# Kernel tuning notes

Hardware: AMD Instinct MI355X
Metric: run time of the kernel (lower is better)

## Reference

```python
import jax, jax.numpy as jnp
import numpy as np


def setup_inputs() -> dict:
    key = jax.random.key(0)
    k1, k2 = jax.random.split(key)
    B, L, V, D = 8, 2048, 1024, 1024
    hidden_states = jax.random.normal(k1, (B, L, D), dtype=jnp.float32)
    visual_hidden_state = jax.random.normal(k2, (B, V, D), dtype=jnp.float32)
    return {"hidden_states": hidden_states, "visual_hidden_state": visual_hidden_state}


def reference(hidden_states, visual_hidden_state):
    # fusion_scores = H @ V^T  (no scaling, no masking)
    scores = jnp.einsum("bld,bvd->blv", hidden_states, visual_hidden_state)
    probs = jax.nn.softmax(scores, axis=-1)
    # fusion_output = probs @ V
    return jnp.einsum("blv,bvd->bld", probs, visual_hidden_state)
```

## Files before the change

kernel.cpp:

```cpp
#include <hip/hip_runtime.h>


typedef _Float16 half8_t __attribute__((ext_vector_type(8)));
typedef _Float16 half4_t __attribute__((ext_vector_type(4)));
typedef __fp16   fp16x2  __attribute__((ext_vector_type(2)));
typedef float    f32x4   __attribute__((ext_vector_type(4)));

#define B_ 8
#define L_ 2048
#define V_ 1024
#define D_ 1024

__device__ __forceinline__ half8_t cvt8(f32x4 a, f32x4 b) {
  union { half8_t h; fp16x2 p[4]; } u;
  u.p[0] = __builtin_amdgcn_cvt_pkrtz(a[0], a[1]);
  u.p[1] = __builtin_amdgcn_cvt_pkrtz(a[2], a[3]);
  u.p[2] = __builtin_amdgcn_cvt_pkrtz(b[0], b[1]);
  u.p[3] = __builtin_amdgcn_cvt_pkrtz(b[2], b[3]);
  return u.h;
}
__device__ __forceinline__ half4_t cvt4(f32x4 a) {
  union { half4_t h; fp16x2 p[2]; } u;
  u.p[0] = __builtin_amdgcn_cvt_pkrtz(a[0], a[1]);
  u.p[1] = __builtin_amdgcn_cvt_pkrtz(a[2], a[3]);
  return u.h;
}

__device__ __forceinline__ void gload_lds16(const _Float16* g, _Float16* l) {
  __builtin_amdgcn_global_load_lds(
      (const __attribute__((address_space(1))) unsigned int*)(g),
      (__attribute__((address_space(3))) unsigned int*)(l), 16, 0, 0);
}

__global__ __launch_bounds__(256) void p0_hconv(const float* __restrict__ H,
                                                _Float16* __restrict__ Hh) {
  const size_t i = ((size_t)blockIdx.x * 256 + threadIdx.x) * 8;
  f32x4 a = *(const f32x4*)(H + i);
  f32x4 b = *(const f32x4*)(H + i + 4);
  *(half8_t*)(Hh + i) = cvt8(a, b);
}

__global__ __launch_bounds__(256) void p1_vconv(const float* __restrict__ V,
                                                _Float16* __restrict__ Vh,
                                                _Float16* __restrict__ VTh) {
  const int b  = blockIdx.z;
  const int d0 = blockIdx.x * 64;
  const int v0 = blockIdx.y * 64;
  const float* Vb = V + (size_t)b * V_ * D_;
  __shared__ __align__(16) _Float16 Lt[64 * 80];
  const int t   = threadIdx.x;
  const int dc4 = (t & 15) * 4;
  #pragma unroll
  for (int it = 0; it < 4; ++it) {
    const int vr = (t >> 4) + it * 16;
    f32x4 x = *(const f32x4*)(Vb + (size_t)(v0 + vr) * D_ + d0 + dc4);
    half4_t h = cvt4(x);
    *(half4_t*)(Vh + (size_t)b * V_ * D_ + (size_t)(v0 + vr) * D_ + d0 + dc4) = h;
    #pragma unroll
    for (int j = 0; j < 4; ++j) Lt[(dc4 + j) * 80 + vr] = h[j];
  }
  __syncthreads();
  #pragma unroll
  for (int it = 0; it < 2; ++it) {
    const int dr = (t >> 3) + it * 32;
    const int vc = (t & 7) * 8;
    half8_t y = *(const half8_t*)&Lt[dr * 80 + vc];
    *(half8_t*)(VTh + (size_t)b * D_ * V_ + (size_t)(d0 + dr) * V_ + v0 + vc) = y;
  }
}

#define BARRIER() asm volatile("s_barrier" ::: "memory")

__global__ __launch_bounds__(512, 2) void gemm256(
    const _Float16* __restrict__ A, const _Float16* __restrict__ B,
    float* __restrict__ C) {
  int lin = blockIdx.x;
  lin = (lin & 7) * 32 + (lin >> 3);
  const int bz = lin >> 5;
  const int my = (lin >> 2) & 7;
  const int nx = lin & 3;
  const int m0 = my * 256, n0 = nx * 256;

  const _Float16* Ap = A + (size_t)bz * (2048 * 1024) + (size_t)m0 * 1024;
  const _Float16* Bp = B + (size_t)bz * (1024 * 1024) + (size_t)n0 * 1024;
  float*          Cp = C + (size_t)bz * (2048 * 1024);

  __shared__ __align__(16) _Float16 As[2][16384];
  __shared__ __align__(16) _Float16 Bs[2][16384];

  const int t    = threadIdx.x;
  const int lane = t & 63;
  const int wid  = t >> 6;
  const int wm   = wid >> 2;
  const int wn   = wid & 3;
  const int fr   = lane & 15;
  const int fk   = lane >> 4;

  f32x4 acc[8][4];
  {
    f32x4 z = {0.f, 0.f, 0.f, 0.f};
    #pragma unroll
    for (int i = 0; i < 8; ++i)
      #pragma unroll
      for (int j = 0; j < 4; ++j) acc[i][j] = z;
  }

  #define STG(PTR, LDSB, H, U)                                                 \
    {                                                                          \
      _Pragma("unroll")                                                        \
      for (int i_ = 0; i_ < 2; ++i_) {                                         \
        const int c_ = i_ * 512 + t;                                           \
        const int kg_ = c_ >> 7, r_ = c_ & 127;                                \
        gload_lds16(PTR + (size_t)((H) * 128 + r_) * 1024 + (U) * 64 + kg_ * 8,\
                    &LDSB[(U) & 1][(kg_ * 256 + (H) * 128 + r_) * 8]);         \
      }                                                                        \
    }

  #define LDA_(mt_, ks_) \
    (*(const half8_t*)&As[buf][(((ks_) * 4 + fk) * 256 + wm * 128 + (mt_) * 16 + fr) * 8])
  #define LDB_(nt_, ks_) \
    (*(const half8_t*)&Bs[buf][(((ks_) * 4 + fk) * 256 + wn * 64 + (nt_) * 16 + fr) * 8])

  #define MFMA16(AF, BF, MOFF, NOFF)                                           \
    __builtin_amdgcn_s_setprio(1);                                             \
    _Pragma("unroll")                                                          \
    for (int ks = 0; ks < 2; ++ks)                                             \
      _Pragma("unroll")                                                        \
      for (int nt = 0; nt < 2; ++nt)                                           \
        _Pragma("unroll")                                                      \
        for (int mt = 0; mt < 4; ++mt)                                         \
          acc[(MOFF) + mt][(NOFF) + nt] =                                      \
              __builtin_amdgcn_mfma_f32_16x16x32_f16(                          \
                  AF[mt][ks], BF[nt][ks], acc[(MOFF) + mt][(NOFF) + nt], 0, 0, 0); \
    __builtin_amdgcn_s_setprio(0);

  STG(Bp, Bs, 0, 0) STG(Ap, As, 0, 0) STG(Bp, Bs, 1, 0) STG(Ap, As, 1, 0)
  STG(Bp, Bs, 0, 1) STG(Ap, As, 0, 1)
  asm volatile("s_waitcnt vmcnt(4)" ::: "memory");
  BARRIER();

  for (int kt = 0; kt < 16; ++kt) {
    const int buf = kt & 1;
    half8_t a0[4][2], b0[2][2], b1[2][2];

    #pragma unroll
    for (int ks = 0; ks < 2; ++ks) {
      #pragma unroll
      for (int mt = 0; mt < 4; ++mt) a0[mt][ks] = LDA_(mt, ks);
      #pragma unroll
      for (int nt = 0; nt < 2; ++nt) b0[nt][ks] = LDB_(nt, ks);
    }
    if (kt + 1 < 16) { STG(Bp, Bs, 1, kt + 1) }
    BARRIER();
    MFMA16(a0, b0, 0, 0)
    BARRIER();

    #pragma unroll
    for (int ks = 0; ks < 2; ++ks)
      #pragma unroll
      for (int nt = 0; nt < 2; ++nt) b1[nt][ks] = LDB_(2 + nt, ks);
    if (kt + 1 < 16) { STG(Ap, As, 1, kt + 1) }
    BARRIER();
    MFMA16(a0, b1, 0, 2)
    BARRIER();

    #pragma unroll
    for (int ks = 0; ks < 2; ++ks)
      #pragma unroll
      for (int mt = 0; mt < 4; ++mt) a0[mt][ks] = LDA_(4 + mt, ks);
    if (kt + 2 < 16) { STG(Bp, Bs, 0, kt + 2) }
    BARRIER();
    MFMA16(a0, b1, 4, 2)
    BARRIER();

    if (kt + 2 < 16) { STG(Ap, As, 0, kt + 2) }
    BARRIER();
    MFMA16(a0, b0, 4, 0)
    if (kt < 14) {
      asm volatile("s_waitcnt vmcnt(4)" ::: "memory");
    } else if (kt == 14) {
      asm volatile("s_waitcnt vmcnt(0)" ::: "memory");
    }
    BARRIER();
  }
  #undef STG
  #undef LDA_
  #undef LDB_
  #undef MFMA16

  const int rq = (lane >> 4) * 4;
  const int cb = n0 + wn * 64 + (lane & 15);
  const int rb = m0 + wm * 128 + rq;
  #pragma unroll
  for (int mt = 0; mt < 8; ++mt)
    #pragma unroll
    for (int nt = 0; nt < 4; ++nt) {
      #pragma unroll
      for (int r = 0; r < 4; ++r)
        Cp[(size_t)(rb + mt * 16 + r) * 1024 + cb + nt * 16] = acc[mt][nt][r];
    }
}

__global__ __launch_bounds__(256) void k2_softmax(const float* __restrict__ S,
                                                  _Float16* __restrict__ P) {
  const int t    = threadIdx.x;
  const int lane = t & 63;
  const int row  = blockIdx.x * 4 + (t >> 6);
  const float* Sr = S + (size_t)row * V_;

  f32x4 s[4];
  #pragma unroll
  for (int j = 0; j < 4; ++j) s[j] = *(const f32x4*)(Sr + (lane + 64 * j) * 4);

  float m = -1e30f;
  #pragma unroll
  for (int j = 0; j < 4; ++j)
    m = fmaxf(m, fmaxf(fmaxf(s[j][0], s[j][1]), fmaxf(s[j][2], s[j][3])));
  #pragma unroll
  for (int off = 1; off < 64; off <<= 1) m = fmaxf(m, __shfl_xor(m, off, 64));

  float sum = 0.f;
  #pragma unroll
  for (int j = 0; j < 4; ++j) {
    s[j][0] = __expf(s[j][0] - m); s[j][1] = __expf(s[j][1] - m);
    s[j][2] = __expf(s[j][2] - m); s[j][3] = __expf(s[j][3] - m);
    sum += (s[j][0] + s[j][1]) + (s[j][2] + s[j][3]);
  }
  #pragma unroll
  for (int off = 1; off < 64; off <<= 1) sum += __shfl_xor(sum, off, 64);
  const float inv = 1.0f / sum;

  _Float16* Pr = P + (size_t)row * V_;
  #pragma unroll
  for (int j = 0; j < 4; ++j) {
    f32x4 e = {s[j][0] * inv, s[j][1] * inv, s[j][2] * inv, s[j][3] * inv};
    *(half4_t*)(Pr + (lane + 64 * j) * 4) = cvt4(e);
  }
}

__global__ __launch_bounds__(256, 2) void k1_slow(
    const float* __restrict__ H, const float* __restrict__ Vv, float* __restrict__ S) {
  const int b  = blockIdx.z;
  const int m0 = blockIdx.y * 128;
  const int n0 = blockIdx.x * 128;
  const float* Hb = H  + (size_t)b * L_ * D_;
  const float* Vb = Vv + (size_t)b * V_ * D_;
  float*       Sb = S  + (size_t)b * L_ * V_;
  __shared__ __align__(16) _Float16 As[2][4096];
  __shared__ __align__(16) _Float16 Bs[2][4096];
  const int t = threadIdx.x, lane = t & 63, wm = (t >> 6) >> 1, wn = (t >> 6) & 1;
  f32x4 acc[4][4];
  { f32x4 z = {0,0,0,0};
    #pragma unroll
    for (int i = 0; i < 4; ++i)
      #pragma unroll
      for (int j = 0; j < 4; ++j) acc[i][j] = z; }
  const int skg = t & 3, sm = t >> 2;
  for (int kt = 0; kt < 32; ++kt) {
    const int kbase = kt * 32 + skg * 8, buf = kt & 1;
    #pragma unroll
    for (int h = 0; h < 2; ++h) {
      const int m = sm + h * 64;
      const float* sa = Hb + (size_t)(m0 + m) * D_ + kbase;
      const float* sb = Vb + (size_t)(n0 + m) * D_ + kbase;
      const int cell = skg * 128 + (m ^ (skg * 2));
      *(half8_t*)&As[buf][cell * 8] = cvt8(*(const f32x4*)sa, *(const f32x4*)(sa + 4));
      *(half8_t*)&Bs[buf][cell * 8] = cvt8(*(const f32x4*)sb, *(const f32x4*)(sb + 4));
    }
    __syncthreads();
    const int fkg = lane >> 4, fr = lane & 15;
    half8_t af[4];
    #pragma unroll
    for (int mt = 0; mt < 4; ++mt)
      af[mt] = *(const half8_t*)&As[buf][(fkg * 128 + ((wm * 64 + mt * 16 + fr) ^ (fkg * 2))) * 8];
    #pragma unroll
    for (int nt = 0; nt < 4; ++nt) {
      half8_t bf = *(const half8_t*)&Bs[buf][(fkg * 128 + ((wn * 64 + nt * 16 + fr) ^ (fkg * 2))) * 8];
      #pragma unroll
      for (int mt = 0; mt < 4; ++mt)
        acc[mt][nt] = __builtin_amdgcn_mfma_f32_16x16x32_f16(af[mt], bf, acc[mt][nt], 0, 0, 0);
    }
  }
  const int rq = (lane >> 4) * 4;
  #pragma unroll
  for (int mt = 0; mt < 4; ++mt)
    #pragma unroll
    for (int nt = 0; nt < 4; ++nt) {
      const int col = n0 + wn * 64 + nt * 16 + (lane & 15);
      const int rb  = m0 + wm * 64 + mt * 16 + rq;
      #pragma unroll
      for (int r = 0; r < 4; ++r) Sb[(size_t)(rb + r) * V_ + col] = acc[mt][nt][r];
    }
}

__global__ __launch_bounds__(256) void k2_slow(float* __restrict__ S) {
  const int row = blockIdx.x;
  float* Sr = S + (size_t)row * V_;
  const int t = threadIdx.x;
  f32x4 s = ((const f32x4*)Sr)[t];
  float m = fmaxf(fmaxf(s[0], s[1]), fmaxf(s[2], s[3]));
  #pragma unroll
  for (int off = 1; off < 64; off <<= 1) m = fmaxf(m, __shfl_xor(m, off, 64));
  __shared__ float redm[4];
  __shared__ float reds[4];
  const int w = t >> 6;
  if ((t & 63) == 0) redm[w] = m;
  __syncthreads();
  m = fmaxf(fmaxf(redm[0], redm[1]), fmaxf(redm[2], redm[3]));
  const float e0 = __expf(s[0] - m), e1 = __expf(s[1] - m);
  const float e2 = __expf(s[2] - m), e3 = __expf(s[3] - m);
  float sum = (e0 + e1) + (e2 + e3);
  #pragma unroll
  for (int off = 1; off < 64; off <<= 1) sum += __shfl_xor(sum, off, 64);
  if ((t & 63) == 0) reds[w] = sum;
  __syncthreads();
  const float inv = 1.0f / ((reds[0] + reds[1]) + (reds[2] + reds[3]));
  half4_t p;
  p[0] = (_Float16)(e0 * inv); p[1] = (_Float16)(e1 * inv);
  p[2] = (_Float16)(e2 * inv); p[3] = (_Float16)(e3 * inv);
  *(half4_t*)((_Float16*)Sr + 4 * t) = p;
}

__global__ __launch_bounds__(512, 2) void k3_slow(
    const float* __restrict__ Vv, float* __restrict__ O) {
  const int b = blockIdx.y, r0 = blockIdx.x * 64;
  const float* Vb = Vv + (size_t)b * V_ * D_;
  float*       Ob = O  + (size_t)b * L_ * D_;
  const _Float16* Pb = (const _Float16*)Ob;
  __shared__ __align__(16) _Float16 Bs[32768];
  const int t = threadIdx.x, lane = t & 63, w = t >> 6;
  f32x4 acc[4][8];
  { f32x4 z = {0,0,0,0};
    #pragma unroll
    for (int i = 0; i < 4; ++i)
      #pragma unroll
      for (int j = 0; j < 8; ++j) acc[i][j] = z; }
  for (int kt = 0; kt < 32; ++kt) {
    const int v0 = kt * 32;
    #pragma unroll
    for (int i = 0; i < 8; ++i) {
      const int c = t + i * 512, kg = c >> 10, d = c & 1023;
      const float* src = Vb + (size_t)(v0 + kg * 8) * D_ + d;
      f32x4 x0, x1;
      x0[0] = src[0*D_]; x0[1] = src[1*D_]; x0[2] = src[2*D_]; x0[3] = src[3*D_];
      x1[0] = src[4*D_]; x1[1] = src[5*D_]; x1[2] = src[6*D_]; x1[3] = src[7*D_];
      *(half8_t*)&Bs[(kg * 1024 + d) * 8] = cvt8(x0, x1);
    }
    __syncthreads();
    const int fkg = lane >> 4, fr = lane & 15;
    half8_t af[4];
    #pragma unroll
    for (int mt = 0; mt < 4; ++mt)
      af[mt] = *(const half8_t*)(Pb + (size_t)(r0 + mt * 16 + fr) * 2048 + v0 + fkg * 8);
    #pragma unroll
    for (int nt = 0; nt < 8; ++nt) {
      half8_t bf = *(const half8_t*)&Bs[(fkg * 1024 + w * 128 + nt * 16 + fr) * 8];
      #pragma unroll
      for (int mt = 0; mt < 4; ++mt)
        acc[mt][nt] = __builtin_amdgcn_mfma_f32_16x16x32_f16(af[mt], bf, acc[mt][nt], 0, 0, 0);
    }
    __syncthreads();
  }
  const int rq = (lane >> 4) * 4;
  #pragma unroll
  for (int mt = 0; mt < 4; ++mt)
    #pragma unroll
    for (int nt = 0; nt < 8; ++nt) {
      const int col = w * 128 + nt * 16 + (lane & 15);
      const int rb  = r0 + mt * 16 + rq;
      #pragma unroll
      for (int r = 0; r < 4; ++r) Ob[(size_t)(rb + r) * D_ + col] = acc[mt][nt][r];
    }
}

extern "C" void kernel_launch(void* const* d_in, const int* in_sizes, int n_in,
                              void* d_out, int out_size, void* d_ws, size_t ws_size,
                              hipStream_t stream) {
  (void)in_sizes; (void)n_in; (void)out_size;
  const float* H  = (const float*)d_in[0];
  const float* Vv = (const float*)d_in[1];
  float* O = (float*)d_out;

  const size_t need = (size_t)64 * 1024 * 1024;
  if (ws_size >= need && d_ws != nullptr) {
    _Float16* Hh  = (_Float16*)d_ws;
    _Float16* Vh  = Hh + (size_t)B_ * L_ * D_;
    _Float16* VTh = Vh + (size_t)B_ * V_ * D_;
    _Float16* P   = Hh;

    p0_hconv<<<dim3((B_ * L_ * D_) / (256 * 8)), 256, 0, stream>>>(H, Hh);
    p1_vconv<<<dim3(D_ / 64, V_ / 64, B_), 256, 0, stream>>>(Vv, Vh, VTh);
    gemm256<<<dim3(256), 512, 0, stream>>>(Hh, Vh, O);
    k2_softmax<<<dim3(B_ * L_ / 4), 256, 0, stream>>>(O, P);
    gemm256<<<dim3(256), 512, 0, stream>>>(P, VTh, O);
  } else {
    k1_slow<<<dim3(V_ / 128, L_ / 128, B_), 256, 0, stream>>>(H, Vv, O);
    k2_slow<<<dim3(B_ * L_), 256, 0, stream>>>(O);
    k3_slow<<<dim3(L_ / 64, B_), 512, 0, stream>>>(Vv, O);
  }
}
```

Measured before the change: 274.2 us.

## Deepen GEMM prefetch to two K-tiles and unroll loop by buffer parity

```diff
diff --git a/kernel.cpp b/kernel.cpp
--- a/kernel.cpp
+++ b/kernel.cpp
@@ -69,7 +69,7 @@
   }
 }
 
-#define BARRIER() asm volatile("s_barrier" ::: "memory")
+#define PH_BAR() asm volatile("s_barrier" ::: "memory")
 
 __global__ __launch_bounds__(512, 2) void gemm256(
     const _Float16* __restrict__ A, const _Float16* __restrict__ B,
@@ -105,21 +105,21 @@
       for (int j = 0; j < 4; ++j) acc[i][j] = z;
   }
 
-  #define STG(PTR, LDSB, H, U)                                                 \
+  #define STG(PTR, ARR, BUFL, H, KTT)                                          \
     {                                                                          \
       _Pragma("unroll")                                                        \
       for (int i_ = 0; i_ < 2; ++i_) {                                         \
         const int c_ = i_ * 512 + t;                                           \
         const int kg_ = c_ >> 7, r_ = c_ & 127;                                \
-        gload_lds16(PTR + (size_t)((H) * 128 + r_) * 1024 + (U) * 64 + kg_ * 8,\
-                    &LDSB[(U) & 1][(kg_ * 256 + (H) * 128 + r_) * 8]);         \
+        gload_lds16(PTR + (size_t)((H) * 128 + r_) * 1024 + (KTT) * 64 + kg_ * 8, \
+                    &ARR[BUFL][(kg_ * 256 + (H) * 128 + r_) * 8]);             \
       }                                                                        \
     }
 
-  #define LDA_(mt_, ks_) \
-    (*(const half8_t*)&As[buf][(((ks_) * 4 + fk) * 256 + wm * 128 + (mt_) * 16 + fr) * 8])
-  #define LDB_(nt_, ks_) \
-    (*(const half8_t*)&Bs[buf][(((ks_) * 4 + fk) * 256 + wn * 64 + (nt_) * 16 + fr) * 8])
+  #define LDA(BUFL, mt_, ks_) \
+    (*(const half8_t*)&As[BUFL][(((ks_) * 4 + fk) * 256 + wm * 128 + (mt_) * 16 + fr) * 8])
+  #define LDB(BUFL, nt_, ks_) \
+    (*(const half8_t*)&Bs[BUFL][(((ks_) * 4 + fk) * 256 + wn * 64 + (nt_) * 16 + fr) * 8])
 
   #define MFMA16(AF, BF, MOFF, NOFF)                                           \
     __builtin_amdgcn_s_setprio(1);                                             \
@@ -134,58 +134,64 @@
                   AF[mt][ks], BF[nt][ks], acc[(MOFF) + mt][(NOFF) + nt], 0, 0, 0); \
     __builtin_amdgcn_s_setprio(0);
 
-  STG(Bp, Bs, 0, 0) STG(Ap, As, 0, 0) STG(Bp, Bs, 1, 0) STG(Ap, As, 1, 0)
-  STG(Bp, Bs, 0, 1) STG(Ap, As, 0, 1)
-  asm volatile("s_waitcnt vmcnt(4)" ::: "memory");
-  BARRIER();
-
-  for (int kt = 0; kt < 16; ++kt) {
-    const int buf = kt & 1;
-    half8_t a0[4][2], b0[2][2], b1[2][2];
-
-    #pragma unroll
-    for (int ks = 0; ks < 2; ++ks) {
-      #pragma unroll
-      for (int mt = 0; mt < 4; ++mt) a0[mt][ks] = LDA_(mt, ks);
-      #pragma unroll
-      for (int nt = 0; nt < 2; ++nt) b0[nt][ks] = LDB_(nt, ks);
-    }
-    if (kt + 1 < 16) { STG(Bp, Bs, 1, kt + 1) }
-    BARRIER();
-    MFMA16(a0, b0, 0, 0)
-    BARRIER();
-
-    #pragma unroll
-    for (int ks = 0; ks < 2; ++ks)
-      #pragma unroll
-      for (int nt = 0; nt < 2; ++nt) b1[nt][ks] = LDB_(2 + nt, ks);
-    if (kt + 1 < 16) { STG(Ap, As, 1, kt + 1) }
-    BARRIER();
-    MFMA16(a0, b1, 0, 2)
-    BARRIER();
-
-    #pragma unroll
-    for (int ks = 0; ks < 2; ++ks)
-      #pragma unroll
-      for (int mt = 0; mt < 4; ++mt) a0[mt][ks] = LDA_(4 + mt, ks);
-    if (kt + 2 < 16) { STG(Bp, Bs, 0, kt + 2) }
-    BARRIER();
-    MFMA16(a0, b1, 4, 2)
-    BARRIER();
-
-    if (kt + 2 < 16) { STG(Ap, As, 0, kt + 2) }
-    BARRIER();
-    MFMA16(a0, b0, 4, 0)
-    if (kt < 14) {
-      asm volatile("s_waitcnt vmcnt(4)" ::: "memory");
-    } else if (kt == 14) {
-      asm volatile("s_waitcnt vmcnt(0)" ::: "memory");
-    }
-    BARRIER();
-  }
+  #define TILE(KT, BUFL)                                                       \
+    {                                                                          \
+      half8_t a[4][2], b0[2][2], b1[2][2];                                     \
+                         \
+      _Pragma("unroll")                                                        \
+      for (int ks = 0; ks < 2; ++ks) {                                         \
+        _Pragma("unroll")                                                      \
+        for (int mt = 0; mt < 4; ++mt) a[mt][ks] = LDA(BUFL, mt, ks);          \
+        _Pragma("unroll")                                                      \
+        for (int nt = 0; nt < 2; ++nt) b0[nt][ks] = LDB(BUFL, nt, ks);         \
+      }                                                                        \
+      PH_BAR();                                                                \
+      MFMA16(a, b0, 0, 0)                                                      \
+      PH_BAR();                                                                \
+                   \
+      _Pragma("unroll")                                                        \
+      for (int ks = 0; ks < 2; ++ks)                                           \
+        _Pragma("unroll")                                                      \
+        for (int nt = 0; nt < 2; ++nt) b1[nt][ks] = LDB(BUFL, 2 + nt, ks);     \
+      if ((KT) < 14) { STG(Bp, Bs, BUFL, 0, (KT) + 2) }                        \
+      PH_BAR();                                                                \
+      MFMA16(a, b1, 0, 2)                                                      \
+      PH_BAR();                                                                \
+                   \
+      _Pragma("unroll")                                                        \
+      for (int ks = 0; ks < 2; ++ks)                                           \
+        _Pragma("unroll")                                                      \
+        for (int mt = 0; mt < 4; ++mt) a[mt][ks] = LDA(BUFL, 4 + mt, ks);      \
+      if ((KT) < 14) { STG(Bp, Bs, BUFL, 1, (KT) + 2) }                        \
+      PH_BAR();                                                                \
+      MFMA16(a, b1, 4, 2)                                                      \
+      PH_BAR();                                                                \
+                \
+      if ((KT) < 14) { STG(Ap, As, BUFL, 0, (KT) + 2) STG(Ap, As, BUFL, 1, (KT) + 2) } \
+      PH_BAR();                                                                \
+      MFMA16(a, b0, 4, 0)                                                      \
+      if ((KT) <= 13) {                                                        \
+        asm volatile("s_waitcnt vmcnt(8)" ::: "memory");                       \
+      } else if ((KT) == 14) {                                                 \
+        asm volatile("s_waitcnt vmcnt(0)" ::: "memory");                       \
+      }                                                                        \
+      PH_BAR();                                                                \
+    }
+
+  STG(Bp, Bs, 0, 0, 0) STG(Ap, As, 0, 0, 0) STG(Bp, Bs, 0, 1, 0) STG(Ap, As, 0, 1, 0)
+  STG(Bp, Bs, 1, 0, 1) STG(Ap, As, 1, 0, 1) STG(Bp, Bs, 1, 1, 1) STG(Ap, As, 1, 1, 1)
+  asm volatile("s_waitcnt vmcnt(8)" ::: "memory");
+  PH_BAR();
+
+  #pragma unroll 1
+  for (int ktp = 0; ktp < 8; ++ktp) {
+    TILE(2 * ktp, 0)
+    TILE(2 * ktp + 1, 1)
+  }
+  #undef TILE
   #undef STG
-  #undef LDA_
-  #undef LDB_
+  #undef LDA
+  #undef LDB
   #undef MFMA16
 
   const int rq = (lane >> 4) * 4;
```

Result: faster. 255.0 us (-7.0%).
